# Performance work log

Measured on AMD Instinct MI355X. Metric: run time of the kernel, lower is better.

Reference implementation:

```python
import jax, jax.numpy as jnp
import numpy as np

B, S, P, D = 256, 2048, 64, 80

def setup_inputs() -> dict:
    key = jax.random.key(0)
    k1, k2, k3, k4 = jax.random.split(key, 4)
    enc_out = jax.random.normal(k1, (B, S, D), dtype=jnp.float32)
    dec_out = jax.random.normal(k2, (B, P, D), dtype=jnp.float32)
    attn_mask = jax.random.randint(k3, (B, S), 0, 2) > 0  # True = masked
    # guarantee at least one unmasked position per row (avoid NaN softmax)
    attn_mask = attn_mask.at[:, 0].set(False)
    W = jax.random.normal(k4, (D, D), dtype=jnp.float32) * (1.0 / np.sqrt(D))
    return {"enc_out": enc_out, "dec_out": dec_out, "attn_mask": attn_mask, "W": W}

def reference(enc_out, dec_out, attn_mask, W):
    # query = Linear(dec_out) with no bias: y = x @ W^T
    query = jnp.einsum('bpd,ed->bpe', dec_out, W)          # (B, P, D)
    # unscaled attention scores (no 1/sqrt(d) in original)
    weight = jnp.einsum('bpd,bsd->bps', query, enc_out)    # (B, P, S)
    neg = jnp.finfo(weight.dtype).min
    weight = jnp.where(attn_mask[:, None, :], neg, weight)
    weight = jax.nn.softmax(weight, axis=-1)
    context = jnp.einsum('bps,bsd->bpd', weight, enc_out)  # (B, P, D)
    return context
```

## Files before the change

kernel.cpp:

```cpp
#include <hip/hip_runtime.h>

#define NB 256
#define NS 2048
#define NP 64
#define ND 80
#define STILE 128
#define NTILE 16
#define NTHREADS 1024
#define LOG2E 1.4426950408889634f

typedef __attribute__((ext_vector_type(4))) float f32x4;
typedef __attribute__((ext_vector_type(2))) __fp16 fp16x2;
typedef __attribute__((ext_vector_type(8))) _Float16 f16x8;
typedef __attribute__((ext_vector_type(4))) unsigned short u16x4;
typedef unsigned short u16;

#define SMEM_BYTES 60944

__device__ __forceinline__ float E2(float x) { return __builtin_amdgcn_exp2f(x); }
__device__ __forceinline__ unsigned pkh(float lo, float hi) {
  union { fp16x2 h; unsigned u; } cv;
  cv.h = __builtin_amdgcn_cvt_pkrtz(lo, hi);
  return cv.u;
}

__device__ __forceinline__ f32x4 mfma16f(f16x8 a, f16x8 b, f32x4 c) {
  return __builtin_amdgcn_mfma_f32_16x16x32_f16(a, b, c, 0, 0, 0);
}

__global__ __launch_bounds__(NTHREADS, 4)
void DecoderAttention_62989990363717_kernel(const float* __restrict__ enc,
                                            const float* __restrict__ dec,
                                            const int* __restrict__ maskp,
                                            const float* __restrict__ W,
                                            float* __restrict__ out)
{
  __shared__ __align__(16) char smem[SMEM_BYTES];

  u16* ehP    = (u16*)smem;
  float* mbias = (float*)(smem + 50688);
  float* mst  = (float*)(smem + 58880);
  float* lst  = (float*)(smem + 59904);
  int* modep  = (int*)(smem + 60928);

  const int tid  = (int)threadIdx.x;
  const int lane = tid & 63;
  const int wv   = tid >> 6;
  const int pp   = wv & 3;
  const int sq   = wv >> 2;
  const int l15  = lane & 15;
  const int g    = lane >> 4;
  const int b    = (int)blockIdx.x;

  const float* encB = enc + (size_t)b * NS * ND;
  const float* decB = dec + (size_t)b * NP * ND;

  {
    float* Wl = (float*)smem;
    float* dl = (float*)(smem + 26880);
    for (int i = tid; i < 80 * 80; i += NTHREADS) Wl[(i / 80) * 84 + (i % 80)] = W[i];
    for (int i = tid; i < 64 * 80; i += NTHREADS)
      dl[(i / 80) * 84 + (i % 80)] = decB[i] * LOG2E;
    if (tid == 0) {
      const unsigned* mw = (const unsigned*)maskp;
      int ok = 1;
      for (int i = 0; i < 16; ++i) ok &= (mw[i] <= 1u);
      *modep = ok;
    }
    __syncthreads();
    const int m32 = *modep;
    if (m32) {
      int v0 = maskp[(size_t)b * NS + tid];
      int v1 = maskp[(size_t)b * NS + tid + 1024];
      mbias[tid]        = v0 ? -3.0e38f : 0.0f;
      mbias[tid + 1024] = v1 ? -3.0e38f : 0.0f;
    } else if (tid < 512) {
      unsigned w = ((const unsigned*)maskp)[(size_t)b * (NS / 4) + tid];
      f32x4 bb;
      bb[0] = (w & 255u)         ? -3.0e38f : 0.0f;
      bb[1] = ((w >> 8) & 255u)  ? -3.0e38f : 0.0f;
      bb[2] = ((w >> 16) & 255u) ? -3.0e38f : 0.0f;
      bb[3] = (w >> 24)          ? -3.0e38f : 0.0f;
      *(f32x4*)&mbias[4 * tid] = bb;
    }
    float qa[5];
    const int qp = tid & 63, qw = tid >> 6;
#pragma unroll
    for (int j = 0; j < 5; ++j) qa[j] = 0.f;
    for (int kg = 0; kg < 20; ++kg) {
      f32x4 dv = *(const f32x4*)&dl[qp * 84 + kg * 4];
#pragma unroll
      for (int j = 0; j < 5; ++j) {
        f32x4 wv4 = *(const f32x4*)&Wl[(qw * 5 + j) * 84 + kg * 4];
        qa[j] = fmaf(dv.x, wv4.x, qa[j]);
        qa[j] = fmaf(dv.y, wv4.y, qa[j]);
        qa[j] = fmaf(dv.z, wv4.z, qa[j]);
        qa[j] = fmaf(dv.w, wv4.w, qa[j]);
      }
    }
    __syncthreads();
    float* qtmp = (float*)smem;
#pragma unroll
    for (int j = 0; j < 5; ++j) qtmp[qp * 100 + qw * 5 + j] = qa[j];
    if (qw == 15) {
#pragma unroll
      for (int z = 0; z < 16; ++z) qtmp[qp * 100 + 80 + z] = 0.f;
    }
    __syncthreads();
  }

  f16x8 qb[3];
  {
    const float* qtmp = (const float*)smem;
    const int prow = 16 * pp + l15;
#pragma unroll
    for (int kk = 0; kk < 3; ++kk) {
      const int d0 = kk * 32 + g * 8;
      f32x4 f0 = *(const f32x4*)&qtmp[prow * 100 + d0];
      f32x4 f1 = *(const f32x4*)&qtmp[prow * 100 + d0 + 4];
      union { _Float16 h[8]; f16x8 v; } H;
      H.h[0] = (_Float16)f0.x; H.h[1] = (_Float16)f0.y;
      H.h[2] = (_Float16)f0.z; H.h[3] = (_Float16)f0.w;
      H.h[4] = (_Float16)f1.x; H.h[5] = (_Float16)f1.y;
      H.h[6] = (_Float16)f1.z; H.h[7] = (_Float16)f1.w;
      qb[kk] = H.v;
    }
  }
  __syncthreads();

  if (tid < 256) {
    const int buf = tid >> 7, q = (tid >> 4) & 7, row = tid & 15;
    u16* p = ehP + buf * 12672 + (q * 6 + 5) * 264 + row * 16;
    *(uint4*)p = make_uint4(0u, 0u, 0u, 0u);
    *(uint4*)(p + 8) = make_uint4(0u, 0u, 0u, 0u);
  }

  const bool ldr = (tid < 640);
  const int srow = tid / 5;
  const int c    = tid - srow * 5;
  u16* ePW = ehP + ((srow >> 4) * 6 + c) * 264 + (srow & 15) * 16;
  const float* gsrc = encB + srow * ND + 16 * c;

#define STAGE_WRITE(bi)                                                          \
  do {                                                                           \
    if (ldr) {                                                                   \
      unsigned hh[8];                                                            \
      hh[0] = pkh(r0.x, r0.y); hh[1] = pkh(r0.z, r0.w);                          \
      hh[2] = pkh(r1.x, r1.y); hh[3] = pkh(r1.z, r1.w);                          \
      hh[4] = pkh(r2.x, r2.y); hh[5] = pkh(r2.z, r2.w);                          \
      hh[6] = pkh(r3.x, r3.y); hh[7] = pkh(r3.z, r3.w);                          \
      u16* a_ = ePW + (bi) * 12672;                                              \
      *(uint4*)a_       = make_uint4(hh[0], hh[1], hh[2], hh[3]);                \
      *(uint4*)(a_ + 8) = make_uint4(hh[4], hh[5], hh[6], hh[7]);                \
    }                                                                            \
  } while (0)

  {
    f32x4 r0, r1, r2, r3;
    if (ldr) {
      r0 = *(const f32x4*)gsrc;       r1 = *(const f32x4*)(gsrc + 4);
      r2 = *(const f32x4*)(gsrc + 8); r3 = *(const f32x4*)(gsrc + 12);
    }
    STAGE_WRITE(0);
    __syncthreads();
  }

  f32x4 ctx[5];
#pragma unroll
  for (int n = 0; n < 5; ++n) ctx[n] = (f32x4){0.f, 0.f, 0.f, 0.f};
  float mr = -1.0e30f, lr = 0.f;

  const int qkOff = (2 * sq) * 1584 + (g >> 1) * 264 + 16 * l15 + 8 * (g & 1);
  const unsigned trBase = (unsigned)(uintptr_t)ehP + (unsigned)(sq * 6336 + 8 * lane);

  for (int tt = 0; tt < NTILE; ++tt) {
    const int cur = tt & 1, nxt = cur ^ 1;
    const bool hn = (tt + 1 < NTILE);
    f32x4 r0, r1, r2, r3;
    if (hn && ldr) {
      const float* src = gsrc + (size_t)(tt + 1) * STILE * ND;
      r0 = *(const f32x4*)src;       r1 = *(const f32x4*)(src + 4);
      r2 = *(const f32x4*)(src + 8); r3 = *(const f32x4*)(src + 12);
    }

    f32x4 a0 = (f32x4){0.f, 0.f, 0.f, 0.f}, a1 = (f32x4){0.f, 0.f, 0.f, 0.f};
    {
      const u16* baseH0 = ehP + cur * 12672 + qkOff;
      const u16* baseH1 = baseH0 + 1584;
      f16x8 e0[3], e1[3];
#pragma unroll
      for (int kk = 0; kk < 3; ++kk) {
        e0[kk] = *(const f16x8*)(const void*)(baseH0 + kk * 528);
        e1[kk] = *(const f16x8*)(const void*)(baseH1 + kk * 528);
      }
#pragma unroll
      for (int kk = 0; kk < 3; ++kk) {
        a0 = mfma16f(e0[kk], qb[kk], a0);
        a1 = mfma16f(e1[kk], qb[kk], a1);
      }
    }

    const int mb0 = tt * 128 + 32 * sq + 4 * g;
    f32x4 bias0 = *(const f32x4*)&mbias[mb0];
    f32x4 bias1 = *(const f32x4*)&mbias[mb0 + 16];
    float sv0[4], sv1[4];
#pragma unroll
    for (int rr = 0; rr < 4; ++rr) {
      sv0[rr] = a0[rr] + bias0[rr];
      sv1[rr] = a1[rr] + bias1[rr];
    }
    float tm = fmaxf(fmaxf(fmaxf(sv0[0], sv0[1]), fmaxf(sv0[2], sv0[3])),
                     fmaxf(fmaxf(sv1[0], sv1[1]), fmaxf(sv1[2], sv1[3])));
    tm = fmaxf(tm, __shfl_xor(tm, 16));
    tm = fmaxf(tm, __shfl_xor(tm, 32));
    const bool need = !__all(tm <= mr + 11.541560f);
    if (need) {
      float mn = fmaxf(mr, tm);
      float esc = E2(mr - mn);
      lr *= esc; mr = mn;
      float fr[4];
#pragma unroll
      for (int rr = 0; rr < 4; ++rr) fr[rr] = __shfl(esc, 4 * g + rr);
#pragma unroll
      for (int n = 0; n < 5; ++n) {
#pragma unroll
        for (int rr = 0; rr < 4; ++rr) ctx[n][rr] *= fr[rr];
      }
    }
    float p0[4], p1[4];
#pragma unroll
    for (int rr = 0; rr < 4; ++rr) {
      p0[rr] = E2(sv0[rr] - mr);
      p1[rr] = E2(sv1[rr] - mr);
    }
    lr += ((p0[0] + p0[1]) + (p0[2] + p0[3])) + ((p1[0] + p1[1]) + (p1[2] + p1[3]));

    union { unsigned uu[4]; f16x8 v; } PA;
    PA.uu[0] = pkh(p0[0], p0[1]); PA.uu[1] = pkh(p0[2], p0[3]);
    PA.uu[2] = pkh(p1[0], p1[1]); PA.uu[3] = pkh(p1[2], p1[3]);
    const unsigned tra = trBase + (unsigned)(cur * 25344);
    {
      u16x4 ta0, tb0, ta1, tb1, ta2, tb2;
      asm volatile("ds_read_b64_tr_b16 %0, %1"             : "=v"(ta0) : "v"(tra));
      asm volatile("ds_read_b64_tr_b16 %0, %1 offset:3168" : "=v"(tb0) : "v"(tra));
      asm volatile("ds_read_b64_tr_b16 %0, %1 offset:528"  : "=v"(ta1) : "v"(tra));
      asm volatile("ds_read_b64_tr_b16 %0, %1 offset:3696" : "=v"(tb1) : "v"(tra));
      asm volatile("ds_read_b64_tr_b16 %0, %1 offset:1056" : "=v"(ta2) : "v"(tra));
      asm volatile("ds_read_b64_tr_b16 %0, %1 offset:4224" : "=v"(tb2) : "v"(tra));
      asm volatile("s_waitcnt lgkmcnt(0)" ::: "memory");
      __builtin_amdgcn_sched_barrier(0);
      union { u16 s[8]; f16x8 v; } B0, B1, B2;
#pragma unroll
      for (int j = 0; j < 4; ++j) {
        B0.s[j] = ta0[j]; B0.s[4 + j] = tb0[j];
        B1.s[j] = ta1[j]; B1.s[4 + j] = tb1[j];
        B2.s[j] = ta2[j]; B2.s[4 + j] = tb2[j];
      }
      ctx[0] = mfma16f(PA.v, B0.v, ctx[0]);
      ctx[1] = mfma16f(PA.v, B1.v, ctx[1]);
      ctx[2] = mfma16f(PA.v, B2.v, ctx[2]);
    }
    {
      u16x4 ta3, tb3, ta4, tb4;
      asm volatile("ds_read_b64_tr_b16 %0, %1 offset:1584" : "=v"(ta3) : "v"(tra));
      asm volatile("ds_read_b64_tr_b16 %0, %1 offset:4752" : "=v"(tb3) : "v"(tra));
      asm volatile("ds_read_b64_tr_b16 %0, %1 offset:2112" : "=v"(ta4) : "v"(tra));
      asm volatile("ds_read_b64_tr_b16 %0, %1 offset:5280" : "=v"(tb4) : "v"(tra));
      asm volatile("s_waitcnt lgkmcnt(0)" ::: "memory");
      __builtin_amdgcn_sched_barrier(0);
      union { u16 s[8]; f16x8 v; } B3, B4;
#pragma unroll
      for (int j = 0; j < 4; ++j) {
        B3.s[j] = ta3[j]; B3.s[4 + j] = tb3[j];
        B4.s[j] = ta4[j]; B4.s[4 + j] = tb4[j];
      }
      ctx[3] = mfma16f(PA.v, B3.v, ctx[3]);
      ctx[4] = mfma16f(PA.v, B4.v, ctx[4]);
    }

    if (hn) { STAGE_WRITE(nxt); }
    __syncthreads();
  }

  lr += __shfl_xor(lr, 16);
  lr += __shfl_xor(lr, 32);
  if (g == 0) {
    mst[sq * 64 + 16 * pp + l15] = mr;
    lst[sq * 64 + 16 * pp + l15] = lr;
  }
  __syncthreads();
  float F;
  {
    const int pi = 16 * pp + l15;
    float M = fmaxf(fmaxf(mst[pi], mst[64 + pi]), fmaxf(mst[128 + pi], mst[192 + pi]));
    F = E2(mr - M);
  }
  float gg[4];
#pragma unroll
  for (int rr = 0; rr < 4; ++rr) gg[rr] = __shfl(F, 4 * g + rr);
  float* cacc = (float*)smem;
  for (int qq = 0; qq < 4; ++qq) {
    if (sq == qq) {
#pragma unroll
      for (int n = 0; n < 5; ++n) {
#pragma unroll
        for (int rr = 0; rr < 4; ++rr) {
          const int row = 16 * pp + 4 * g + rr;
          const int col = 16 * n + l15;
          float v = ctx[n][rr] * gg[rr];
          if (qq == 0) cacc[row * 84 + col] = v;
          else         cacc[row * 84 + col] += v;
        }
      }
    }
    __syncthreads();
  }
  {
    const int op = tid >> 4, oc = tid & 15;
    float Mv = fmaxf(fmaxf(mst[op], mst[64 + op]), fmaxf(mst[128 + op], mst[192 + op]));
    float Lv = lst[op] * E2(mst[op] - Mv) + lst[64 + op] * E2(mst[64 + op] - Mv)
             + lst[128 + op] * E2(mst[128 + op] - Mv) + lst[192 + op] * E2(mst[192 + op] - Mv);
    float inv = 1.0f / Lv;
    float* orow = out + ((size_t)b * NP + op) * ND + oc * 5;
    const float* crow = cacc + op * 84 + oc * 5;
#pragma unroll
    for (int i = 0; i < 5; ++i) orow[i] = crow[i] * inv;
  }
}

extern "C" void kernel_launch(void* const* d_in, const int* in_sizes, int n_in,
                              void* d_out, int out_size, void* d_ws, size_t ws_size,
                              hipStream_t stream) {
  (void)in_sizes; (void)n_in; (void)out_size; (void)d_ws; (void)ws_size;
  const float* enc  = (const float*)d_in[0];
  const float* dec  = (const float*)d_in[1];
  const int*   mask = (const int*)d_in[2];
  const float* W    = (const float*)d_in[3];
  float* out = (float*)d_out;
  DecoderAttention_62989990363717_kernel<<<dim3(NB), dim3(NTHREADS), 0, stream>>>(
      enc, dec, mask, W, out);
}
```

Before: 40.23 us.

## Split each batch's query rows across two blocks of 512 threads

Launches two blocks per batch element, each handling 32 of the 64 query rows with 512 threads instead of one 1024-thread block handling all 64. This doubles the grid to 512 blocks so more CUs are occupied on a chip with 256 CUs. The cost is that each encoder tile is loaded and converted to fp16 twice, once per block, which doubles global reads of enc. Loader indexing, mask setup, Q projection mapping and the final reduction offsets are adjusted for the smaller block.

After: 64.60 us. 60.6% more time.

```diff
diff --git a/kernel.cpp b/kernel.cpp
--- a/kernel.cpp
+++ b/kernel.cpp
@@ -1,12 +1,11 @@
 #include <hip/hip_runtime.h>
 
-#define NB 256
 #define NS 2048
 #define NP 64
 #define ND 80
 #define STILE 128
 #define NTILE 16
-#define NTHREADS 1024
+#define NTHREADS 512
 #define LOG2E 1.4426950408889634f
 
 typedef __attribute__((ext_vector_type(4))) float f32x4;
@@ -23,7 +22,6 @@
   cv.h = __builtin_amdgcn_cvt_pkrtz(lo, hi);
   return cv.u;
 }
-
 __device__ __forceinline__ f32x4 mfma16f(f16x8 a, f16x8 b, f32x4 c) {
   return __builtin_amdgcn_mfma_f32_16x16x32_f16(a, b, c, 0, 0, 0);
 }
@@ -46,20 +44,21 @@
   const int tid  = (int)threadIdx.x;
   const int lane = tid & 63;
   const int wv   = tid >> 6;
-  const int pp   = wv & 3;
-  const int sq   = wv >> 2;
+  const int pp   = wv & 1;
+  const int sq   = wv >> 1;
   const int l15  = lane & 15;
   const int g    = lane >> 4;
-  const int b    = (int)blockIdx.x;
-
-  const float* encB = enc + (size_t)b * NS * ND;
-  const float* decB = dec + (size_t)b * NP * ND;
+  const int bb   = (int)blockIdx.x >> 1;
+  const int phB  = (int)blockIdx.x & 1;
+
+  const float* encB = enc + (size_t)bb * NS * ND;
+  const float* decB = dec + ((size_t)bb * NP + 32 * phB) * ND;
 
   {
     float* Wl = (float*)smem;
     float* dl = (float*)(smem + 26880);
     for (int i = tid; i < 80 * 80; i += NTHREADS) Wl[(i / 80) * 84 + (i % 80)] = W[i];
-    for (int i = tid; i < 64 * 80; i += NTHREADS)
+    for (int i = tid; i < 32 * 80; i += NTHREADS)
       dl[(i / 80) * 84 + (i % 80)] = decB[i] * LOG2E;
     if (tid == 0) {
       const unsigned* mw = (const unsigned*)maskp;
@@ -70,21 +69,22 @@
     __syncthreads();
     const int m32 = *modep;
     if (m32) {
-      int v0 = maskp[(size_t)b * NS + tid];
-      int v1 = maskp[(size_t)b * NS + tid + 1024];
-      mbias[tid]        = v0 ? -3.0e38f : 0.0f;
-      mbias[tid + 1024] = v1 ? -3.0e38f : 0.0f;
-    } else if (tid < 512) {
-      unsigned w = ((const unsigned*)maskp)[(size_t)b * (NS / 4) + tid];
-      f32x4 bb;
-      bb[0] = (w & 255u)         ? -3.0e38f : 0.0f;
-      bb[1] = ((w >> 8) & 255u)  ? -3.0e38f : 0.0f;
-      bb[2] = ((w >> 16) & 255u) ? -3.0e38f : 0.0f;
-      bb[3] = (w >> 24)          ? -3.0e38f : 0.0f;
-      *(f32x4*)&mbias[4 * tid] = bb;
+#pragma unroll
+      for (int k = 0; k < 4; ++k) {
+        int v = maskp[(size_t)bb * NS + tid + 512 * k];
+        mbias[tid + 512 * k] = v ? -3.0e38f : 0.0f;
+      }
+    } else {
+      unsigned w = ((const unsigned*)maskp)[(size_t)bb * (NS / 4) + tid];
+      f32x4 bv;
+      bv[0] = (w & 255u)         ? -3.0e38f : 0.0f;
+      bv[1] = ((w >> 8) & 255u)  ? -3.0e38f : 0.0f;
+      bv[2] = ((w >> 16) & 255u) ? -3.0e38f : 0.0f;
+      bv[3] = (w >> 24)          ? -3.0e38f : 0.0f;
+      *(f32x4*)&mbias[4 * tid] = bv;
     }
     float qa[5];
-    const int qp = tid & 63, qw = tid >> 6;
+    const int qp = tid >> 4, qw = tid & 15;
 #pragma unroll
     for (int j = 0; j < 5; ++j) qa[j] = 0.f;
     for (int kg = 0; kg < 20; ++kg) {
@@ -135,31 +135,38 @@
     *(uint4*)(p + 8) = make_uint4(0u, 0u, 0u, 0u);
   }
 
-  const bool ldr = (tid < 640);
-  const int srow = tid / 5;
-  const int c    = tid - srow * 5;
-  u16* ePW = ehP + ((srow >> 4) * 6 + c) * 264 + (srow & 15) * 16;
-  const float* gsrc = encB + srow * ND + 16 * c;
+  const int rowA = tid / 5, cA = tid - rowA * 5;
+  u16* ePWa = ehP + ((rowA >> 4) * 6 + cA) * 264 + (rowA & 15) * 16;
+  const float* gsrcA = encB + rowA * ND + 16 * cA;
+  const bool ldrB = (tid < 128);
+  const int chB = 512 + tid, rowB = chB / 5, cB = chB - rowB * 5;
+  u16* ePWb = ehP + ((rowB >> 4) * 6 + cB) * 264 + (rowB & 15) * 16;
+  const float* gsrcB = encB + rowB * ND + 16 * cB;
+
+#define PACK16(dst, q0, q1, q2, q3)                                              \
+  do {                                                                           \
+    unsigned hh[8];                                                              \
+    hh[0] = pkh(q0.x, q0.y); hh[1] = pkh(q0.z, q0.w);                            \
+    hh[2] = pkh(q1.x, q1.y); hh[3] = pkh(q1.z, q1.w);                            \
+    hh[4] = pkh(q2.x, q2.y); hh[5] = pkh(q2.z, q2.w);                            \
+    hh[6] = pkh(q3.x, q3.y); hh[7] = pkh(q3.z, q3.w);                            \
+    *(uint4*)(dst)       = make_uint4(hh[0], hh[1], hh[2], hh[3]);               \
+    *(uint4*)((dst) + 8) = make_uint4(hh[4], hh[5], hh[6], hh[7]);               \
+  } while (0)
 
 #define STAGE_WRITE(bi)                                                          \
   do {                                                                           \
-    if (ldr) {                                                                   \
-      unsigned hh[8];                                                            \
-      hh[0] = pkh(r0.x, r0.y); hh[1] = pkh(r0.z, r0.w);                          \
-      hh[2] = pkh(r1.x, r1.y); hh[3] = pkh(r1.z, r1.w);                          \
-      hh[4] = pkh(r2.x, r2.y); hh[5] = pkh(r2.z, r2.w);                          \
-      hh[6] = pkh(r3.x, r3.y); hh[7] = pkh(r3.z, r3.w);                          \
-      u16* a_ = ePW + (bi) * 12672;                                              \
-      *(uint4*)a_       = make_uint4(hh[0], hh[1], hh[2], hh[3]);                \
-      *(uint4*)(a_ + 8) = make_uint4(hh[4], hh[5], hh[6], hh[7]);                \
-    }                                                                            \
+    PACK16(ePWa + (bi) * 12672, rA0, rA1, rA2, rA3);                             \
+    if (ldrB) { PACK16(ePWb + (bi) * 12672, rB0, rB1, rB2, rB3); }               \
   } while (0)
 
   {
-    f32x4 r0, r1, r2, r3;
-    if (ldr) {
-      r0 = *(const f32x4*)gsrc;       r1 = *(const f32x4*)(gsrc + 4);
-      r2 = *(const f32x4*)(gsrc + 8); r3 = *(const f32x4*)(gsrc + 12);
+    f32x4 rA0 = *(const f32x4*)gsrcA,       rA1 = *(const f32x4*)(gsrcA + 4);
+    f32x4 rA2 = *(const f32x4*)(gsrcA + 8), rA3 = *(const f32x4*)(gsrcA + 12);
+    f32x4 rB0, rB1, rB2, rB3;
+    if (ldrB) {
+      rB0 = *(const f32x4*)gsrcB;       rB1 = *(const f32x4*)(gsrcB + 4);
+      rB2 = *(const f32x4*)(gsrcB + 8); rB3 = *(const f32x4*)(gsrcB + 12);
     }
     STAGE_WRITE(0);
     __syncthreads();
@@ -176,11 +183,16 @@
   for (int tt = 0; tt < NTILE; ++tt) {
     const int cur = tt & 1, nxt = cur ^ 1;
     const bool hn = (tt + 1 < NTILE);
-    f32x4 r0, r1, r2, r3;
-    if (hn && ldr) {
-      const float* src = gsrc + (size_t)(tt + 1) * STILE * ND;
-      r0 = *(const f32x4*)src;       r1 = *(const f32x4*)(src + 4);
-      r2 = *(const f32x4*)(src + 8); r3 = *(const f32x4*)(src + 12);
+    f32x4 rA0, rA1, rA2, rA3, rB0, rB1, rB2, rB3;
+    if (hn) {
+      const float* sA = gsrcA + (size_t)(tt + 1) * STILE * ND;
+      rA0 = *(const f32x4*)sA;       rA1 = *(const f32x4*)(sA + 4);
+      rA2 = *(const f32x4*)(sA + 8); rA3 = *(const f32x4*)(sA + 12);
+      if (ldrB) {
+        const float* sB = gsrcB + (size_t)(tt + 1) * STILE * ND;
+        rB0 = *(const f32x4*)sB;       rB1 = *(const f32x4*)(sB + 4);
+        rB2 = *(const f32x4*)(sB + 8); rB3 = *(const f32x4*)(sB + 12);
+      }
     }
 
     f32x4 a0 = (f32x4){0.f, 0.f, 0.f, 0.f}, a1 = (f32x4){0.f, 0.f, 0.f, 0.f};
@@ -285,14 +297,14 @@
   lr += __shfl_xor(lr, 16);
   lr += __shfl_xor(lr, 32);
   if (g == 0) {
-    mst[sq * 64 + 16 * pp + l15] = mr;
-    lst[sq * 64 + 16 * pp + l15] = lr;
+    mst[sq * 32 + 16 * pp + l15] = mr;
+    lst[sq * 32 + 16 * pp + l15] = lr;
   }
   __syncthreads();
   float F;
   {
     const int pi = 16 * pp + l15;
-    float M = fmaxf(fmaxf(mst[pi], mst[64 + pi]), fmaxf(mst[128 + pi], mst[192 + pi]));
+    float M = fmaxf(fmaxf(mst[pi], mst[32 + pi]), fmaxf(mst[64 + pi], mst[96 + pi]));
     F = E2(mr - M);
   }
   float gg[4];
@@ -317,11 +329,11 @@
   }
   {
     const int op = tid >> 4, oc = tid & 15;
-    float Mv = fmaxf(fmaxf(mst[op], mst[64 + op]), fmaxf(mst[128 + op], mst[192 + op]));
-    float Lv = lst[op] * E2(mst[op] - Mv) + lst[64 + op] * E2(mst[64 + op] - Mv)
-             + lst[128 + op] * E2(mst[128 + op] - Mv) + lst[192 + op] * E2(mst[192 + op] - Mv);
+    float Mv = fmaxf(fmaxf(mst[op], mst[32 + op]), fmaxf(mst[64 + op], mst[96 + op]));
+    float Lv = lst[op] * E2(mst[op] - Mv) + lst[32 + op] * E2(mst[32 + op] - Mv)
+             + lst[64 + op] * E2(mst[64 + op] - Mv) + lst[96 + op] * E2(mst[96 + op] - Mv);
     float inv = 1.0f / Lv;
-    float* orow = out + ((size_t)b * NP + op) * ND + oc * 5;
+    float* orow = out + ((size_t)bb * NP + 32 * phB + op) * ND + oc * 5;
     const float* crow = cacc + op * 84 + oc * 5;
 #pragma unroll
     for (int i = 0; i < 5; ++i) orow[i] = crow[i] * inv;
@@ -337,6 +349,6 @@
   const int*   mask = (const int*)d_in[2];
   const float* W    = (const float*)d_in[3];
   float* out = (float*)d_out;
-  DecoderAttention_62989990363717_kernel<<<dim3(NB), dim3(NTHREADS), 0, stream>>>(
+  DecoderAttention_62989990363717_kernel<<<dim3(512), dim3(NTHREADS), 0, stream>>>(
       enc, dec, mask, W, out);
 }
```

## Split sequence across two blocks per batch with flash-decoding style merge kernel

Applied to the files above, without the earlier changes.

Adds a split-S path: 512 blocks of 512 threads each process half the encoder sequence for one batch. Each block writes a normalized fp16 partial context plus max and sum statistics to workspace, and a second kernel merges the two halves. The goal is more blocks and finer-grained parallelism per CU. The cost is a second launch, workspace traffic, and fp16 rounding of the partial outputs. The LDS transpose reads are also issued all together before the softmax so they overlap with it, applied to both paths, and the original monolithic kernel is kept as a fallback when the workspace is too small.

Result: slower. 48.20 us (+19.8%).

```diff
diff --git a/kernel.cpp b/kernel.cpp
--- a/kernel.cpp
+++ b/kernel.cpp
@@ -1,12 +1,8 @@
 #include <hip/hip_runtime.h>
 
-#define NB 256
 #define NS 2048
 #define NP 64
 #define ND 80
-#define STILE 128
-#define NTILE 16
-#define NTHREADS 1024
 #define LOG2E 1.4426950408889634f
 
 typedef __attribute__((ext_vector_type(4))) float f32x4;
@@ -14,8 +10,6 @@
 typedef __attribute__((ext_vector_type(8))) _Float16 f16x8;
 typedef __attribute__((ext_vector_type(4))) unsigned short u16x4;
 typedef unsigned short u16;
-
-#define SMEM_BYTES 60944
 
 __device__ __forceinline__ float E2(float x) { return __builtin_amdgcn_exp2f(x); }
 __device__ __forceinline__ unsigned pkh(float lo, float hi) {
@@ -23,20 +17,346 @@
   cv.h = __builtin_amdgcn_cvt_pkrtz(lo, hi);
   return cv.u;
 }
-
+__device__ __forceinline__ float f16f(u16 v) {
+  union { u16 u; _Float16 h; } c; c.u = v; return (float)c.h;
+}
 __device__ __forceinline__ f32x4 mfma16f(f16x8 a, f16x8 b, f32x4 c) {
   return __builtin_amdgcn_mfma_f32_16x16x32_f16(a, b, c, 0, 0, 0);
 }
 
-__global__ __launch_bounds__(NTHREADS, 4)
-void DecoderAttention_62989990363717_kernel(const float* __restrict__ enc,
-                                            const float* __restrict__ dec,
-                                            const int* __restrict__ maskp,
-                                            const float* __restrict__ W,
-                                            float* __restrict__ out)
+#define SP_SMEM 57616
+
+__global__ __launch_bounds__(512, 4)
+void da_split(const float* __restrict__ enc, const float* __restrict__ dec,
+              const int* __restrict__ maskp, const float* __restrict__ W,
+              u16* __restrict__ wsO, float* __restrict__ wsM,
+              float* __restrict__ wsL)
 {
-  __shared__ __align__(16) char smem[SMEM_BYTES];
-
+  __shared__ __align__(16) char smem[SP_SMEM];
+  u16* ehP    = (u16*)smem;
+  float* mbias = (float*)(smem + 25600);
+  float* mst  = (float*)(smem + 29696);
+  float* lst  = (float*)(smem + 30208);
+  int* modep  = (int*)(smem + 30720);
+
+  const int tid  = (int)threadIdx.x;
+  const int lane = tid & 63;
+  const int wv   = tid >> 6;
+  const int pp   = wv & 3;
+  const int sq   = wv >> 2;
+  const int l15  = lane & 15;
+  const int g    = lane >> 4;
+  const int bid  = (int)blockIdx.x;
+  const int bb   = bid >> 1;
+  const int sh   = bid & 1;
+
+  const float* encB = enc + ((size_t)bb * NS + 1024 * sh) * ND;
+  const float* decB = dec + (size_t)bb * NP * ND;
+
+  {
+    float* Wl = (float*)(smem + 30736);
+    float* dl = (float*)smem;
+    for (int i = tid; i < 80 * 80; i += 512) Wl[(i / 80) * 84 + (i % 80)] = W[i];
+    for (int i = tid; i < 64 * 80; i += 512)
+      dl[(i / 80) * 84 + (i % 80)] = decB[i] * LOG2E;
+    if (tid == 0) {
+      const unsigned* mw = (const unsigned*)maskp;
+      int ok = 1;
+      for (int i = 0; i < 16; ++i) ok &= (mw[i] <= 1u);
+      *modep = ok;
+    }
+    __syncthreads();
+    const int m32 = *modep;
+    if (m32) {
+      int v0 = maskp[(size_t)bb * NS + 1024 * sh + tid];
+      int v1 = maskp[(size_t)bb * NS + 1024 * sh + tid + 512];
+      mbias[tid]       = v0 ? -3.0e38f : 0.0f;
+      mbias[tid + 512] = v1 ? -3.0e38f : 0.0f;
+    } else if (tid < 256) {
+      unsigned w = ((const unsigned*)maskp)[(size_t)bb * (NS / 4) + 256 * sh + tid];
+      f32x4 bv;
+      bv[0] = (w & 255u)         ? -3.0e38f : 0.0f;
+      bv[1] = ((w >> 8) & 255u)  ? -3.0e38f : 0.0f;
+      bv[2] = ((w >> 16) & 255u) ? -3.0e38f : 0.0f;
+      bv[3] = (w >> 24)          ? -3.0e38f : 0.0f;
+      *(f32x4*)&mbias[4 * tid] = bv;
+    }
+    float qa[10];
+    const int qp = tid & 63, qw = tid >> 6;
+#pragma unroll
+    for (int j = 0; j < 10; ++j) qa[j] = 0.f;
+    for (int kg = 0; kg < 20; ++kg) {
+      f32x4 dv = *(const f32x4*)&dl[qp * 84 + kg * 4];
+#pragma unroll
+      for (int j = 0; j < 10; ++j) {
+        f32x4 wv4 = *(const f32x4*)&Wl[(qw * 10 + j) * 84 + kg * 4];
+        qa[j] = fmaf(dv.x, wv4.x, qa[j]);
+        qa[j] = fmaf(dv.y, wv4.y, qa[j]);
+        qa[j] = fmaf(dv.z, wv4.z, qa[j]);
+        qa[j] = fmaf(dv.w, wv4.w, qa[j]);
+      }
+    }
+    __syncthreads();
+    float* qtmp = (float*)smem;
+#pragma unroll
+    for (int j = 0; j < 10; ++j) qtmp[qp * 100 + qw * 10 + j] = qa[j];
+    if (qw == 7) {
+#pragma unroll
+      for (int z = 0; z < 16; ++z) qtmp[qp * 100 + 80 + z] = 0.f;
+    }
+    __syncthreads();
+  }
+
+  f16x8 qb[3];
+  {
+    const float* qtmp = (const float*)smem;
+    const int prow = 16 * pp + l15;
+#pragma unroll
+    for (int kk = 0; kk < 3; ++kk) {
+      const int d0 = kk * 32 + g * 8;
+      f32x4 f0 = *(const f32x4*)&qtmp[prow * 100 + d0];
+      f32x4 f1 = *(const f32x4*)&qtmp[prow * 100 + d0 + 4];
+      union { _Float16 h[8]; f16x8 v; } H;
+      H.h[0] = (_Float16)f0.x; H.h[1] = (_Float16)f0.y;
+      H.h[2] = (_Float16)f0.z; H.h[3] = (_Float16)f0.w;
+      H.h[4] = (_Float16)f1.x; H.h[5] = (_Float16)f1.y;
+      H.h[6] = (_Float16)f1.z; H.h[7] = (_Float16)f1.w;
+      qb[kk] = H.v;
+    }
+  }
+  __syncthreads();
+
+  if (tid < 128) {
+    const int buf = tid >> 6, q = (tid >> 4) & 3, row = tid & 15;
+    u16* p = ehP + buf * 6336 + (q * 6 + 5) * 264 + row * 16;
+    *(uint4*)p = make_uint4(0u, 0u, 0u, 0u);
+    *(uint4*)(p + 8) = make_uint4(0u, 0u, 0u, 0u);
+  }
+
+  const bool ldr = (tid < 320);
+  const int srow = tid / 5;
+  const int c    = tid - srow * 5;
+  u16* ePW = ehP + ((srow >> 4) * 6 + c) * 264 + (srow & 15) * 16;
+  const float* gsrc = encB + srow * ND + 16 * c;
+
+#define SP_STAGE(bi)                                                             \
+  do {                                                                           \
+    if (ldr) {                                                                   \
+      unsigned hh[8];                                                            \
+      hh[0] = pkh(r0.x, r0.y); hh[1] = pkh(r0.z, r0.w);                          \
+      hh[2] = pkh(r1.x, r1.y); hh[3] = pkh(r1.z, r1.w);                          \
+      hh[4] = pkh(r2.x, r2.y); hh[5] = pkh(r2.z, r2.w);                          \
+      hh[6] = pkh(r3.x, r3.y); hh[7] = pkh(r3.z, r3.w);                          \
+      u16* a_ = ePW + (bi) * 6336;                                               \
+      *(uint4*)a_       = make_uint4(hh[0], hh[1], hh[2], hh[3]);                \
+      *(uint4*)(a_ + 8) = make_uint4(hh[4], hh[5], hh[6], hh[7]);                \
+    }                                                                            \
+  } while (0)
+
+  {
+    f32x4 r0, r1, r2, r3;
+    if (ldr) {
+      r0 = *(const f32x4*)gsrc;       r1 = *(const f32x4*)(gsrc + 4);
+      r2 = *(const f32x4*)(gsrc + 8); r3 = *(const f32x4*)(gsrc + 12);
+    }
+    SP_STAGE(0);
+    __syncthreads();
+  }
+
+  f32x4 ctx[5];
+#pragma unroll
+  for (int n = 0; n < 5; ++n) ctx[n] = (f32x4){0.f, 0.f, 0.f, 0.f};
+  float mr = -1.0e30f, lr = 0.f;
+
+  const int qkOff = (2 * sq) * 1584 + (g >> 1) * 264 + 16 * l15 + 8 * (g & 1);
+  const unsigned trBase = (unsigned)(uintptr_t)ehP + (unsigned)(sq * 6336 + 8 * lane);
+
+  for (int tt = 0; tt < 16; ++tt) {
+    const int cur = tt & 1, nxt = cur ^ 1;
+    const bool hn = (tt + 1 < 16);
+    f32x4 r0, r1, r2, r3;
+    if (hn && ldr) {
+      const float* src = gsrc + (size_t)(tt + 1) * 64 * ND;
+      r0 = *(const f32x4*)src;       r1 = *(const f32x4*)(src + 4);
+      r2 = *(const f32x4*)(src + 8); r3 = *(const f32x4*)(src + 12);
+    }
+
+    f32x4 a0 = (f32x4){0.f, 0.f, 0.f, 0.f}, a1 = (f32x4){0.f, 0.f, 0.f, 0.f};
+    {
+      const u16* baseH0 = ehP + cur * 6336 + qkOff;
+      const u16* baseH1 = baseH0 + 1584;
+      f16x8 e0[3], e1[3];
+#pragma unroll
+      for (int kk = 0; kk < 3; ++kk) {
+        e0[kk] = *(const f16x8*)(const void*)(baseH0 + kk * 528);
+        e1[kk] = *(const f16x8*)(const void*)(baseH1 + kk * 528);
+      }
+#pragma unroll
+      for (int kk = 0; kk < 3; ++kk) {
+        a0 = mfma16f(e0[kk], qb[kk], a0);
+        a1 = mfma16f(e1[kk], qb[kk], a1);
+      }
+    }
+
+    const int mb0 = tt * 64 + 32 * sq + 4 * g;
+    f32x4 bias0 = *(const f32x4*)&mbias[mb0];
+    f32x4 bias1 = *(const f32x4*)&mbias[mb0 + 16];
+
+    const unsigned tra = trBase + (unsigned)(cur * 12672);
+    u16x4 ta0, tb0, ta1, tb1, ta2, tb2, ta3, tb3, ta4, tb4;
+    asm volatile("ds_read_b64_tr_b16 %0, %1"             : "=v"(ta0) : "v"(tra));
+    asm volatile("ds_read_b64_tr_b16 %0, %1 offset:3168" : "=v"(tb0) : "v"(tra));
+    asm volatile("ds_read_b64_tr_b16 %0, %1 offset:528"  : "=v"(ta1) : "v"(tra));
+    asm volatile("ds_read_b64_tr_b16 %0, %1 offset:3696" : "=v"(tb1) : "v"(tra));
+    asm volatile("ds_read_b64_tr_b16 %0, %1 offset:1056" : "=v"(ta2) : "v"(tra));
+    asm volatile("ds_read_b64_tr_b16 %0, %1 offset:4224" : "=v"(tb2) : "v"(tra));
+    asm volatile("ds_read_b64_tr_b16 %0, %1 offset:1584" : "=v"(ta3) : "v"(tra));
+    asm volatile("ds_read_b64_tr_b16 %0, %1 offset:4752" : "=v"(tb3) : "v"(tra));
+    asm volatile("ds_read_b64_tr_b16 %0, %1 offset:2112" : "=v"(ta4) : "v"(tra));
+    asm volatile("ds_read_b64_tr_b16 %0, %1 offset:5280" : "=v"(tb4) : "v"(tra));
+
+    float sv0[4], sv1[4];
+#pragma unroll
+    for (int rr = 0; rr < 4; ++rr) {
+      sv0[rr] = a0[rr] + bias0[rr];
+      sv1[rr] = a1[rr] + bias1[rr];
+    }
+    float tm = fmaxf(fmaxf(fmaxf(sv0[0], sv0[1]), fmaxf(sv0[2], sv0[3])),
+                     fmaxf(fmaxf(sv1[0], sv1[1]), fmaxf(sv1[2], sv1[3])));
+    tm = fmaxf(tm, __shfl_xor(tm, 16));
+    tm = fmaxf(tm, __shfl_xor(tm, 32));
+    const bool need = !__all(tm <= mr + 11.541560f);
+    if (need) {
+      float mn = fmaxf(mr, tm);
+      float esc = E2(mr - mn);
+      lr *= esc; mr = mn;
+      float fr[4];
+#pragma unroll
+      for (int rr = 0; rr < 4; ++rr) fr[rr] = __shfl(esc, 4 * g + rr);
+#pragma unroll
+      for (int n = 0; n < 5; ++n) {
+#pragma unroll
+        for (int rr = 0; rr < 4; ++rr) ctx[n][rr] *= fr[rr];
+      }
+    }
+    float p0[4], p1[4];
+#pragma unroll
+    for (int rr = 0; rr < 4; ++rr) {
+      p0[rr] = E2(sv0[rr] - mr);
+      p1[rr] = E2(sv1[rr] - mr);
+    }
+    lr += ((p0[0] + p0[1]) + (p0[2] + p0[3])) + ((p1[0] + p1[1]) + (p1[2] + p1[3]));
+
+    union { unsigned uu[4]; f16x8 v; } PA;
+    PA.uu[0] = pkh(p0[0], p0[1]); PA.uu[1] = pkh(p0[2], p0[3]);
+    PA.uu[2] = pkh(p1[0], p1[1]); PA.uu[3] = pkh(p1[2], p1[3]);
+    asm volatile("s_waitcnt lgkmcnt(0)" ::: "memory");
+    __builtin_amdgcn_sched_barrier(0);
+    {
+      union { u16 s[8]; f16x8 v; } B0, B1, B2, B3, B4;
+#pragma unroll
+      for (int j = 0; j < 4; ++j) {
+        B0.s[j] = ta0[j]; B0.s[4 + j] = tb0[j];
+        B1.s[j] = ta1[j]; B1.s[4 + j] = tb1[j];
+        B2.s[j] = ta2[j]; B2.s[4 + j] = tb2[j];
+        B3.s[j] = ta3[j]; B3.s[4 + j] = tb3[j];
+        B4.s[j] = ta4[j]; B4.s[4 + j] = tb4[j];
+      }
+      ctx[0] = mfma16f(PA.v, B0.v, ctx[0]);
+      ctx[1] = mfma16f(PA.v, B1.v, ctx[1]);
+      ctx[2] = mfma16f(PA.v, B2.v, ctx[2]);
+      ctx[3] = mfma16f(PA.v, B3.v, ctx[3]);
+      ctx[4] = mfma16f(PA.v, B4.v, ctx[4]);
+    }
+
+    if (hn) { SP_STAGE(nxt); }
+    __syncthreads();
+  }
+
+  lr += __shfl_xor(lr, 16);
+  lr += __shfl_xor(lr, 32);
+  if (g == 0) {
+    mst[sq * 64 + 16 * pp + l15] = mr;
+    lst[sq * 64 + 16 * pp + l15] = lr;
+  }
+  __syncthreads();
+  float F;
+  {
+    const int pi = 16 * pp + l15;
+    float M = fmaxf(mst[pi], mst[64 + pi]);
+    F = E2(mr - M);
+  }
+  float gg[4];
+#pragma unroll
+  for (int rr = 0; rr < 4; ++rr) gg[rr] = __shfl(F, 4 * g + rr);
+  float* cacc = (float*)smem;
+  for (int qq = 0; qq < 2; ++qq) {
+    if (sq == qq) {
+#pragma unroll
+      for (int n = 0; n < 5; ++n) {
+#pragma unroll
+        for (int rr = 0; rr < 4; ++rr) {
+          const int row = 16 * pp + 4 * g + rr;
+          const int col = 16 * n + l15;
+          float v = ctx[n][rr] * gg[rr];
+          if (qq == 0) cacc[row * 84 + col] = v;
+          else         cacc[row * 84 + col] += v;
+        }
+      }
+    }
+    __syncthreads();
+  }
+  if (tid < 64) {
+    const int p = tid;
+    float Mv = fmaxf(mst[p], mst[64 + p]);
+    float Lv = lst[p] * E2(mst[p] - Mv) + lst[64 + p] * E2(mst[64 + p] - Mv);
+    wsM[bid * 64 + p] = Mv;
+    wsL[bid * 64 + p] = Lv;
+  }
+  {
+    const int op = tid >> 3, oc = tid & 7;
+    float Mv = fmaxf(mst[op], mst[64 + op]);
+    float Lv = lst[op] * E2(mst[op] - Mv) + lst[64 + op] * E2(mst[64 + op] - Mv);
+    float inv = (Lv > 0.f) ? 1.0f / Lv : 0.f;
+    const float* crow = cacc + op * 84 + oc * 10;
+    u16* dst = wsO + (size_t)bid * 5120 + op * 80 + oc * 10;
+#pragma unroll
+    for (int k = 0; k < 10; k += 2)
+      *(unsigned*)&dst[k] = pkh(crow[k] * inv, crow[k + 1] * inv);
+  }
+}
+
+__global__ __launch_bounds__(512)
+void da_merge(const u16* __restrict__ wsO, const float* __restrict__ wsM,
+              const float* __restrict__ wsL, float* __restrict__ out)
+{
+  const int bb  = (int)blockIdx.x;
+  const int tid = (int)threadIdx.x;
+  const int p   = tid >> 3, i = tid & 7;
+  float mA = wsM[bb * 128 + p],      mB = wsM[bb * 128 + 64 + p];
+  float lA = wsL[bb * 128 + p],      lB = wsL[bb * 128 + 64 + p];
+  float M  = fmaxf(mA, mB);
+  float wA = lA * E2(mA - M), wB = lB * E2(mB - M);
+  float inv = 1.0f / (wA + wB);
+  const u16* a  = wsO + (size_t)(bb * 2) * 5120 + p * 80 + i * 10;
+  const u16* b2 = a + 5120;
+  float* o = out + (size_t)bb * 5120 + p * 80 + i * 10;
+#pragma unroll
+  for (int k = 0; k < 10; k += 2) {
+    float2 v;
+    v.x = (f16f(a[k])     * wA + f16f(b2[k])     * wB) * inv;
+    v.y = (f16f(a[k + 1]) * wA + f16f(b2[k + 1]) * wB) * inv;
+    *(float2*)&o[k] = v;
+  }
+}
+
+#define MO_SMEM 60944
+__global__ __launch_bounds__(1024, 4)
+void da_mono(const float* __restrict__ enc, const float* __restrict__ dec,
+             const int* __restrict__ maskp, const float* __restrict__ W,
+             float* __restrict__ out)
+{
+  __shared__ __align__(16) char smem[MO_SMEM];
   u16* ehP    = (u16*)smem;
   float* mbias = (float*)(smem + 50688);
   float* mst  = (float*)(smem + 58880);
@@ -58,8 +378,8 @@
   {
     float* Wl = (float*)smem;
     float* dl = (float*)(smem + 26880);
-    for (int i = tid; i < 80 * 80; i += NTHREADS) Wl[(i / 80) * 84 + (i % 80)] = W[i];
-    for (int i = tid; i < 64 * 80; i += NTHREADS)
+    for (int i = tid; i < 80 * 80; i += 1024) Wl[(i / 80) * 84 + (i % 80)] = W[i];
+    for (int i = tid; i < 64 * 80; i += 1024)
       dl[(i / 80) * 84 + (i % 80)] = decB[i] * LOG2E;
     if (tid == 0) {
       const unsigned* mw = (const unsigned*)maskp;
@@ -141,7 +461,7 @@
   u16* ePW = ehP + ((srow >> 4) * 6 + c) * 264 + (srow & 15) * 16;
   const float* gsrc = encB + srow * ND + 16 * c;
 
-#define STAGE_WRITE(bi)                                                          \
+#define MO_STAGE(bi)                                                             \
   do {                                                                           \
     if (ldr) {                                                                   \
       unsigned hh[8];                                                            \
@@ -161,7 +481,7 @@
       r0 = *(const f32x4*)gsrc;       r1 = *(const f32x4*)(gsrc + 4);
       r2 = *(const f32x4*)(gsrc + 8); r3 = *(const f32x4*)(gsrc + 12);
     }
-    STAGE_WRITE(0);
+    MO_STAGE(0);
     __syncthreads();
   }
 
@@ -173,12 +493,12 @@
   const int qkOff = (2 * sq) * 1584 + (g >> 1) * 264 + 16 * l15 + 8 * (g & 1);
   const unsigned trBase = (unsigned)(uintptr_t)ehP + (unsigned)(sq * 6336 + 8 * lane);
 
-  for (int tt = 0; tt < NTILE; ++tt) {
+  for (int tt = 0; tt < 16; ++tt) {
     const int cur = tt & 1, nxt = cur ^ 1;
-    const bool hn = (tt + 1 < NTILE);
+    const bool hn = (tt + 1 < 16);
     f32x4 r0, r1, r2, r3;
     if (hn && ldr) {
-      const float* src = gsrc + (size_t)(tt + 1) * STILE * ND;
+      const float* src = gsrc + (size_t)(tt + 1) * 128 * ND;
       r0 = *(const f32x4*)src;       r1 = *(const f32x4*)(src + 4);
       r2 = *(const f32x4*)(src + 8); r3 = *(const f32x4*)(src + 12);
     }
@@ -203,6 +523,20 @@
     const int mb0 = tt * 128 + 32 * sq + 4 * g;
     f32x4 bias0 = *(const f32x4*)&mbias[mb0];
     f32x4 bias1 = *(const f32x4*)&mbias[mb0 + 16];
+
+    const unsigned tra = trBase + (unsigned)(cur * 25344);
+    u16x4 ta0, tb0, ta1, tb1, ta2, tb2, ta3, tb3, ta4, tb4;
+    asm volatile("ds_read_b64_tr_b16 %0, %1"             : "=v"(ta0) : "v"(tra));
+    asm volatile("ds_read_b64_tr_b16 %0, %1 offset:3168" : "=v"(tb0) : "v"(tra));
+    asm volatile("ds_read_b64_tr_b16 %0, %1 offset:528"  : "=v"(ta1) : "v"(tra));
+    asm volatile("ds_read_b64_tr_b16 %0, %1 offset:3696" : "=v"(tb1) : "v"(tra));
+    asm volatile("ds_read_b64_tr_b16 %0, %1 offset:1056" : "=v"(ta2) : "v"(tra));
+    asm volatile("ds_read_b64_tr_b16 %0, %1 offset:4224" : "=v"(tb2) : "v"(tra));
+    asm volatile("ds_read_b64_tr_b16 %0, %1 offset:1584" : "=v"(ta3) : "v"(tra));
+    asm volatile("ds_read_b64_tr_b16 %0, %1 offset:4752" : "=v"(tb3) : "v"(tra));
+    asm volatile("ds_read_b64_tr_b16 %0, %1 offset:2112" : "=v"(ta4) : "v"(tra));
+    asm volatile("ds_read_b64_tr_b16 %0, %1 offset:5280" : "=v"(tb4) : "v"(tra));
+
     float sv0[4], sv1[4];
 #pragma unroll
     for (int rr = 0; rr < 4; ++rr) {
@@ -238,47 +572,26 @@
     union { unsigned uu[4]; f16x8 v; } PA;
     PA.uu[0] = pkh(p0[0], p0[1]); PA.uu[1] = pkh(p0[2], p0[3]);
     PA.uu[2] = pkh(p1[0], p1[1]); PA.uu[3] = pkh(p1[2], p1[3]);
-    const unsigned tra = trBase + (unsigned)(cur * 25344);
+    asm volatile("s_waitcnt lgkmcnt(0)" ::: "memory");
+    __builtin_amdgcn_sched_barrier(0);
     {
-      u16x4 ta0, tb0, ta1, tb1, ta2, tb2;
-      asm volatile("ds_read_b64_tr_b16 %0, %1"             : "=v"(ta0) : "v"(tra));
-      asm volatile("ds_read_b64_tr_b16 %0, %1 offset:3168" : "=v"(tb0) : "v"(tra));
-      asm volatile("ds_read_b64_tr_b16 %0, %1 offset:528"  : "=v"(ta1) : "v"(tra));
-      asm volatile("ds_read_b64_tr_b16 %0, %1 offset:3696" : "=v"(tb1) : "v"(tra));
-      asm volatile("ds_read_b64_tr_b16 %0, %1 offset:1056" : "=v"(ta2) : "v"(tra));
-      asm volatile("ds_read_b64_tr_b16 %0, %1 offset:4224" : "=v"(tb2) : "v"(tra));
-      asm volatile("s_waitcnt lgkmcnt(0)" ::: "memory");
-      __builtin_amdgcn_sched_barrier(0);
-      union { u16 s[8]; f16x8 v; } B0, B1, B2;
+      union { u16 s[8]; f16x8 v; } B0, B1, B2, B3, B4;
 #pragma unroll
       for (int j = 0; j < 4; ++j) {
         B0.s[j] = ta0[j]; B0.s[4 + j] = tb0[j];
         B1.s[j] = ta1[j]; B1.s[4 + j] = tb1[j];
         B2.s[j] = ta2[j]; B2.s[4 + j] = tb2[j];
+        B3.s[j] = ta3[j]; B3.s[4 + j] = tb3[j];
+        B4.s[j] = ta4[j]; B4.s[4 + j] = tb4[j];
       }
       ctx[0] = mfma16f(PA.v, B0.v, ctx[0]);
       ctx[1] = mfma16f(PA.v, B1.v, ctx[1]);
       ctx[2] = mfma16f(PA.v, B2.v, ctx[2]);
-    }
-    {
-      u16x4 ta3, tb3, ta4, tb4;
-      asm volatile("ds_read_b64_tr_b16 %0, %1 offset:1584" : "=v"(ta3) : "v"(tra));
-      asm volatile("ds_read_b64_tr_b16 %0, %1 offset:4752" : "=v"(tb3) : "v"(tra));
-      asm volatile("ds_read_b64_tr_b16 %0, %1 offset:2112" : "=v"(ta4) : "v"(tra));
-      asm volatile("ds_read_b64_tr_b16 %0, %1 offset:5280" : "=v"(tb4) : "v"(tra));
-      asm volatile("s_waitcnt lgkmcnt(0)" ::: "memory");
-      __builtin_amdgcn_sched_barrier(0);
-      union { u16 s[8]; f16x8 v; } B3, B4;
-#pragma unroll
-      for (int j = 0; j < 4; ++j) {
-        B3.s[j] = ta3[j]; B3.s[4 + j] = tb3[j];
-        B4.s[j] = ta4[j]; B4.s[4 + j] = tb4[j];
-      }
       ctx[3] = mfma16f(PA.v, B3.v, ctx[3]);
       ctx[4] = mfma16f(PA.v, B4.v, ctx[4]);
     }
 
-    if (hn) { STAGE_WRITE(nxt); }
+    if (hn) { MO_STAGE(nxt); }
     __syncthreads();
   }
 
@@ -331,12 +644,20 @@
 extern "C" void kernel_launch(void* const* d_in, const int* in_sizes, int n_in,
                               void* d_out, int out_size, void* d_ws, size_t ws_size,
                               hipStream_t stream) {
-  (void)in_sizes; (void)n_in; (void)out_size; (void)d_ws; (void)ws_size;
+  (void)in_sizes; (void)n_in; (void)out_size;
   const float* enc  = (const float*)d_in[0];
   const float* dec  = (const float*)d_in[1];
   const int*   mask = (const int*)d_in[2];
   const float* W    = (const float*)d_in[3];
   float* out = (float*)d_out;
-  DecoderAttention_62989990363717_kernel<<<dim3(NB), dim3(NTHREADS), 0, stream>>>(
-      enc, dec, mask, W, out);
+  const size_t WS_NEEDED = (size_t)512 * 5120 * 2 + (size_t)2 * 512 * 64 * 4;
+  if (ws_size >= WS_NEEDED) {
+    u16* wsO   = (u16*)d_ws;
+    float* wsM = (float*)((char*)d_ws + (size_t)512 * 5120 * 2);
+    float* wsL = wsM + 512 * 64;
+    da_split<<<dim3(512), dim3(512), 0, stream>>>(enc, dec, mask, W, wsO, wsM, wsL);
+    da_merge<<<dim3(256), dim3(512), 0, stream>>>(wsO, wsM, wsL, out);
+  } else {
+    da_mono<<<dim3(256), dim3(1024), 0, stream>>>(enc, dec, mask, W, out);
+  }
 }
```
